# Kernel optimization log

Measured on AMD Instinct MI355X. Metric: run time of the kernel, lower is better.

Reference implementation:

```python
import jax, jax.numpy as jnp
import numpy as np

NUM_QUANTIZERS = 8
CODEBOOK_SIZE = 1024
DIM = 64
B, N = 8, 8192


def setup_inputs() -> dict:
    key = jax.random.key(0)
    kx, kc = jax.random.split(key)
    x = jax.random.normal(kx, (B, N, DIM), dtype=jnp.float32)
    # one codebook per quantizer stage (shared_codebook=False)
    codebooks = jax.random.normal(kc, (NUM_QUANTIZERS, CODEBOOK_SIZE, DIM), dtype=jnp.float32)
    return {"x": x, "codebooks": codebooks}


def reference(x, codebooks):
    """Residual VQ: sequential nearest-codebook lookup with residual subtraction.

    x:         [b, n, d]
    codebooks: [Q, K, d]
    returns quantized_out: [b, n, d]
    """

    def step(carry, cb):
        residual, qout = carry                       # [b,n,d], [b,n,d]
        # squared euclidean distances, [b,n,K]
        r_sq = jnp.sum(residual * residual, axis=-1, keepdims=True)
        c_sq = jnp.sum(cb * cb, axis=-1)             # [K]
        dots = jnp.einsum('bnd,kd->bnk', residual, cb)
        dist = r_sq - 2.0 * dots + c_sq              # [b,n,K]
        idx = jnp.argmin(dist, axis=-1)              # [b,n]
        quant = cb[idx]                              # [b,n,d] gather
        # straight-through estimator (VectorQuantize forward)
        quant_st = residual + jax.lax.stop_gradient(quant - residual)
        new_residual = residual - jax.lax.stop_gradient(quant)
        return (new_residual, qout + quant_st), idx

    init = (x, jnp.zeros_like(x))
    (residual, quantized_out), all_indices = jax.lax.scan(step, init, codebooks)
    return quantized_out
```

## Files before the change

kernel.cpp:

```cpp
#include <hip/hip_runtime.h>

#define NQ 8
#define KCODES 1024
#define D 64
#define CHUNK 64
#define NCHUNK 16
#define TPB 256
#define TOKPB 128
#define BIAS 96.0f

using short8 = __attribute__((ext_vector_type(8))) short;
using f32x4  = __attribute__((ext_vector_type(4))) float;

#define GLOBAL_AS __attribute__((address_space(1)))
#define LDS_AS    __attribute__((address_space(3)))

static __device__ __forceinline__ unsigned bf16_rne_bits(float f) {
    unsigned u = __float_as_uint(f);
    return (u + 0x7fffu + ((u >> 16) & 1u)) >> 16;
}
static __device__ __forceinline__ unsigned umn(unsigned a, unsigned b) { return a < b ? a : b; }
static __device__ __forceinline__ unsigned umx(unsigned a, unsigned b) { return a > b ? a : b; }
static __device__ __forceinline__ unsigned umed3(unsigned a, unsigned b, unsigned c) {
    return umx(umn(a, b), umn(umx(a, b), c));
}

__global__ __launch_bounds__(256) void prep_cb(const float* __restrict__ cb,
                                               int4* __restrict__ ws_cb) {
    int id = blockIdx.x * 256 + threadIdx.x;
    int n_rel = id & 63;
    int plane = (id >> 6) & 15;
    int ch    = (id >> 10) & 15;
    int q     = id >> 14;
    int g = plane & 3, kt = (plane >> 2) & 1, term = plane >> 3;
    int n = ch * CHUNK + n_rel;
    const float* src = cb + ((size_t)(q * KCODES + n)) * D + kt * 32 + g * 8;
    union { short s[8]; int4 v; } u;
    #pragma unroll
    for (int j = 0; j < 8; ++j) {
        float f = -src[j];
        unsigned hb = bf16_rne_bits(f);
        if (term == 0) {
            u.s[j] = (short)hb;
        } else {
            float lo = f - __uint_as_float(hb << 16);
            u.s[j] = (short)bf16_rne_bits(lo);
        }
    }
    ws_cb[id] = u.v;
}

__global__ __launch_bounds__(256) void prep_csq(const float* __restrict__ cb,
                                                float* __restrict__ ws_csq,
                                                float* __restrict__ ws_csqh) {
    int id = blockIdx.x * 256 + threadIdx.x;
    const float* c = cb + (size_t)id * D;
    float s0 = 0.f, s1 = 0.f, s2 = 0.f, s3 = 0.f;
    #pragma unroll
    for (int j = 0; j < 16; ++j) {
        s0 = fmaf(c[4*j+0], c[4*j+0], s0);
        s1 = fmaf(c[4*j+1], c[4*j+1], s1);
        s2 = fmaf(c[4*j+2], c[4*j+2], s2);
        s3 = fmaf(c[4*j+3], c[4*j+3], s3);
    }
    float cs = (s0 + s1) + (s2 + s3);
    ws_csq[id]  = cs;
    ws_csqh[id] = 0.5f * cs + BIAS;
}

__global__ __launch_bounds__(TPB, 4) void rvq_mfma(
    const float* __restrict__ x,
    const float* __restrict__ cb,
    const int4* __restrict__ ws_cb,
    const float* __restrict__ ws_csq,
    float* __restrict__ out)
{
    __shared__ __align__(16) int4  lds_stage[1024];
    __shared__ __align__(16) float lds_resid[TOKPB * 68];
    __shared__ float    lds_csqh[CHUNK];
    __shared__ unsigned lds_cand[TOKPB * 3];
    __shared__ int      lds_pick[TOKPB];

    const int tid  = threadIdx.x;
    const int lane = tid & 63;
    const int wave = tid >> 6;
    const int g    = lane >> 4;
    const int c    = lane & 15;
    const int tok0 = blockIdx.x * TOKPB;

    {
        const int t = tid >> 1, part = tid & 1;
        const float4* xp = (const float4*)(x + (size_t)(tok0 + t) * D + part * 32);
        float4* rr = (float4*)(lds_resid + t * 68 + part * 32);
        #pragma unroll
        for (int k2 = 0; k2 < 8; ++k2) rr[k2] = xp[k2];
    }

    const char* bp = (const char*)lds_stage + (c << 4) + (g << 10);

    for (int q = 0; q < NQ; ++q) {
        __syncthreads();

        short8 ah0[2], ah1[2], al0[2], al1[2];
        #pragma unroll
        for (int s = 0; s < 2; ++s) {
            const float* rr = lds_resid + (wave * 32 + s * 16 + c) * 68;
            float4 f0 = *(const float4*)(rr + 8 * g);
            float4 f1 = *(const float4*)(rr + 8 * g + 4);
            float4 f2 = *(const float4*)(rr + 32 + 8 * g);
            float4 f3 = *(const float4*)(rr + 36 + 8 * g);
            const float* v0 = (const float*)&f0;
            const float* v1 = (const float*)&f1;
            const float* v2 = (const float*)&f2;
            const float* v3 = (const float*)&f3;
            #pragma unroll
            for (int j = 0; j < 4; ++j) {
                float a = v0[j], b = v1[j], e = v2[j], f = v3[j];
                unsigned ha = bf16_rne_bits(a);
                unsigned hb = bf16_rne_bits(b);
                unsigned he = bf16_rne_bits(e);
                unsigned hf = bf16_rne_bits(f);
                ah0[s][j]   = (short)ha;  ah0[s][4+j] = (short)hb;
                ah1[s][j]   = (short)he;  ah1[s][4+j] = (short)hf;
                al0[s][j]   = (short)bf16_rne_bits(a - __uint_as_float(ha << 16));
                al0[s][4+j] = (short)bf16_rne_bits(b - __uint_as_float(hb << 16));
                al1[s][j]   = (short)bf16_rne_bits(e - __uint_as_float(he << 16));
                al1[s][4+j] = (short)bf16_rne_bits(f - __uint_as_float(hf << 16));
            }
        }

        unsigned T1[2][4], T2[2][4], T3[2][4];
        #pragma unroll
        for (int s = 0; s < 2; ++s)
            #pragma unroll
            for (int r = 0; r < 4; ++r) { T1[s][r] = 0xFFFFFFFFu; T2[s][r] = 0xFFFFFFFFu; T3[s][r] = 0xFFFFFFFFu; }

        for (int ch = 0; ch < NCHUNK; ++ch) {
            __syncthreads();
            {
                const int4* src = ws_cb + (size_t)(q * NCHUNK + ch) * 1024 + tid;
                LDS_AS char* ldst = (LDS_AS char*)lds_stage + tid * 16;
                #pragma unroll
                for (int t = 0; t < 4; ++t) {
                    __builtin_amdgcn_global_load_lds(
                        (const GLOBAL_AS unsigned int*)(src + t * 256),
                        (LDS_AS unsigned int*)(ldst + t * 4096), 16, 0, 0);
                }
                if (tid < CHUNK) {
                    __builtin_amdgcn_global_load_lds(
                        (const GLOBAL_AS unsigned int*)(ws_csq + 8192 + q * KCODES + ch * CHUNK + tid),
                        (LDS_AS unsigned int*)(&lds_csqh[tid]), 4, 0, 0);
                }
            }
            __syncthreads();

            #pragma unroll
            for (int tt = 0; tt < 4; ++tt) {
                short8 bh0 = *(const short8*)(bp + tt * 256);
                short8 bh1 = *(const short8*)(bp + 4096  + tt * 256);
                short8 bl0 = *(const short8*)(bp + 8192  + tt * 256);
                short8 bl1 = *(const short8*)(bp + 12288 + tt * 256);
                const float sd = lds_csqh[tt * 16 + c];
                const unsigned codev = (unsigned)(ch * CHUNK + tt * 16 + c);
                #pragma unroll
                for (int s = 0; s < 2; ++s) {
                    f32x4 acc = {sd, sd, sd, sd};
                    acc = __builtin_amdgcn_mfma_f32_16x16x32_bf16(ah0[s], bh0, acc, 0, 0, 0);
                    acc = __builtin_amdgcn_mfma_f32_16x16x32_bf16(ah1[s], bh1, acc, 0, 0, 0);
                    acc = __builtin_amdgcn_mfma_f32_16x16x32_bf16(al0[s], bh0, acc, 0, 0, 0);
                    acc = __builtin_amdgcn_mfma_f32_16x16x32_bf16(ah0[s], bl0, acc, 0, 0, 0);
                    acc = __builtin_amdgcn_mfma_f32_16x16x32_bf16(al1[s], bh1, acc, 0, 0, 0);
                    acc = __builtin_amdgcn_mfma_f32_16x16x32_bf16(ah1[s], bl1, acc, 0, 0, 0);
                    #pragma unroll
                    for (int r = 0; r < 4; ++r) {
                        unsigned p = (__float_as_uint(acc[r]) & 0xFFFFFC00u) | codev;
                        unsigned n2 = umn(T2[s][r], umx(T1[s][r], p));
                        unsigned n3 = umn(T3[s][r], umx(T2[s][r], p));
                        T1[s][r] = umn(T1[s][r], p);
                        T2[s][r] = n2;
                        T3[s][r] = n3;
                    }
                }
            }
        }

        #pragma unroll
        for (int st = 1; st <= 8; st <<= 1) {
            #pragma unroll
            for (int s = 0; s < 2; ++s) {
                #pragma unroll
                for (int r = 0; r < 4; ++r) {
                    unsigned o1 = (unsigned)__shfl_xor((int)T1[s][r], st);
                    unsigned o2 = (unsigned)__shfl_xor((int)T2[s][r], st);
                    unsigned o3 = (unsigned)__shfl_xor((int)T3[s][r], st);
                    unsigned x1 = umn(T1[s][r], o1), y1 = umx(T1[s][r], o1);
                    unsigned x2 = umn(T2[s][r], o2), y2 = umx(T2[s][r], o2);
                    unsigned x3 = umn(T3[s][r], o3);
                    T1[s][r] = x1;
                    T3[s][r] = umed3(y1, x2, umn(y2, x3));
                    T2[s][r] = umn(y1, x2);
                }
            }
        }

        if (c == 0) {
            #pragma unroll
            for (int s = 0; s < 2; ++s)
                #pragma unroll
                for (int r = 0; r < 4; ++r) {
                    const int idx = (wave * 32 + s * 16 + g * 4 + r) * 3;
                    lds_cand[idx + 0] = T1[s][r];
                    lds_cand[idx + 1] = T2[s][r];
                    lds_cand[idx + 2] = T3[s][r];
                }
        }
        __syncthreads();

        #pragma unroll
        for (int p = 0; p < 2; ++p) {
            const int t4  = lane >> 2;
            const int sel = lane & 3;
            const int row = wave * 32 + p * 16 + t4;
            const unsigned m1 = lds_cand[row * 3 + 0];
            const unsigned m2 = lds_cand[row * 3 + 1];
            const unsigned m3 = lds_cand[row * 3 + 2];
            const unsigned psel = (sel == 0) ? m1 : ((sel == 1) ? m2 : m3);
            const int cd = (int)(psel & 1023u);

            const float4* rrv = (const float4*)(lds_resid + row * 68);
            const float4* cpv = (const float4*)(cb + ((size_t)(q * KCODES + cd)) * D);
            float ax = 0.f, ay = 0.f, az = 0.f, aw = 0.f;
            #pragma unroll
            for (int j = 0; j < 16; ++j) {
                float4 rv = rrv[j];
                float4 cv = cpv[j];
                ax = fmaf(rv.x, cv.x, ax);
                ay = fmaf(rv.y, cv.y, ay);
                az = fmaf(rv.z, cv.z, az);
                aw = fmaf(rv.w, cv.w, aw);
            }
            float dot = (ax + ay) + (az + aw);
            float dd = fmaf(dot, -2.0f, ws_csq[q * KCODES + cd]);

            const int base = lane & ~3;
            float d0 = __shfl(dd, base);
            float d1 = __shfl(dd, base + 1);
            float d2 = __shfl(dd, base + 2);
            int cc0 = (int)(m1 & 1023u);
            int cc1 = (int)(m2 & 1023u);
            int cc2 = (int)(m3 & 1023u);
            float db = d0; int pick = cc0;
            if (d1 < db || (d1 == db && cc1 < pick)) { db = d1; pick = cc1; }
            if (d2 < db || (d2 == db && cc2 < pick)) { db = d2; pick = cc2; }
            if (sel == 0) lds_pick[row] = pick;
        }
        __syncthreads();

        {
            const int t = tid >> 1, part = tid & 1;
            const int ifin = lds_pick[t];
            const float4* cp = (const float4*)(cb + ((size_t)(q * KCODES + ifin)) * D + part * 32);
            float4* rr = (float4*)(lds_resid + t * 68 + part * 32);
            #pragma unroll
            for (int k2 = 0; k2 < 8; ++k2) {
                float4 rv = rr[k2], cv = cp[k2];
                rv.x -= cv.x; rv.y -= cv.y; rv.z -= cv.z; rv.w -= cv.w;
                rr[k2] = rv;
            }
        }
    }

    __syncthreads();
    {
        const int t = tid >> 1, part = tid & 1;
        const float4* xp = (const float4*)(x + (size_t)(tok0 + t) * D + part * 32);
        const float4* rr = (const float4*)(lds_resid + t * 68 + part * 32);
        float4* op = (float4*)(out + (size_t)(tok0 + t) * D + part * 32);
        #pragma unroll
        for (int k2 = 0; k2 < 8; ++k2) {
            float4 xv = xp[k2], rv = rr[k2];
            float4 o;
            o.x = xv.x - rv.x; o.y = xv.y - rv.y;
            o.z = xv.z - rv.z; o.w = xv.w - rv.w;
            op[k2] = o;
        }
    }
}

extern "C" void kernel_launch(void* const* d_in, const int* in_sizes, int n_in,
                              void* d_out, int out_size, void* d_ws, size_t ws_size,
                              hipStream_t stream) {
    const float* x  = (const float*)d_in[0];
    const float* cb = (const float*)d_in[1];
    float* out = (float*)d_out;

    int4*  ws_cb   = (int4*)d_ws;
    float* ws_csq  = (float*)((char*)d_ws + (size_t)2 * 1024 * 1024);
    float* ws_csqh = ws_csq + 8192;

    prep_cb <<<512, 256, 0, stream>>>(cb, ws_cb);
    prep_csq<<< 32, 256, 0, stream>>>(cb, ws_csq, ws_csqh);

    const int n_tokens = in_sizes[0] / D;
    const int grid = n_tokens / TOKPB;
    rvq_mfma<<<grid, TPB, 0, stream>>>(x, cb, ws_cb, ws_csq, out);
}
```

Before: 367.5 us.

## Halve tokens per block and split codebook chunk across wave pairs

Each block now handles 64 tokens instead of 128. Pairs of waves share the same 32 tokens, and each wave computes distances against half of every 64-code chunk. Per-half top-3 candidate lists are merged through LDS before the exact fp32 rescoring. This doubles the grid size to give more blocks for occupancy and latency hiding across CUs. In exchange, the codebook staging traffic per token doubles and a merge step is added.

```diff
diff --git a/kernel.cpp b/kernel.cpp
--- a/kernel.cpp
+++ b/kernel.cpp
@@ -6,7 +6,7 @@
 #define CHUNK 64
 #define NCHUNK 16
 #define TPB 256
-#define TOKPB 128
+#define TOKPB 64
 #define BIAS 96.0f
 
 using short8 = __attribute__((ext_vector_type(8))) short;
@@ -78,25 +78,27 @@
     __shared__ __align__(16) int4  lds_stage[1024];
     __shared__ __align__(16) float lds_resid[TOKPB * 68];
     __shared__ float    lds_csqh[CHUNK];
-    __shared__ unsigned lds_cand[TOKPB * 3];
+    __shared__ unsigned lds_cand[2][TOKPB * 3];
     __shared__ int      lds_pick[TOKPB];
 
-    const int tid  = threadIdx.x;
-    const int lane = tid & 63;
-    const int wave = tid >> 6;
-    const int g    = lane >> 4;
-    const int c    = lane & 15;
-    const int tok0 = blockIdx.x * TOKPB;
+    const int tid   = threadIdx.x;
+    const int lane  = tid & 63;
+    const int wave  = tid >> 6;
+    const int group = wave >> 1;
+    const int half  = wave & 1;
+    const int g     = lane >> 4;
+    const int c     = lane & 15;
+    const int tok0  = blockIdx.x * TOKPB;
 
     {
-        const int t = tid >> 1, part = tid & 1;
-        const float4* xp = (const float4*)(x + (size_t)(tok0 + t) * D + part * 32);
-        float4* rr = (float4*)(lds_resid + t * 68 + part * 32);
-        #pragma unroll
-        for (int k2 = 0; k2 < 8; ++k2) rr[k2] = xp[k2];
-    }
-
-    const char* bp = (const char*)lds_stage + (c << 4) + (g << 10);
+        const int t = tid >> 2, part = tid & 3;
+        const float4* xp = (const float4*)(x + (size_t)(tok0 + t) * D + part * 16);
+        float4* rr = (float4*)(lds_resid + t * 68 + part * 16);
+        #pragma unroll
+        for (int k2 = 0; k2 < 4; ++k2) rr[k2] = xp[k2];
+    }
+
+    const char* bp = (const char*)lds_stage + (c << 4) + (g << 10) + half * 512;
 
     for (int q = 0; q < NQ; ++q) {
         __syncthreads();
@@ -104,7 +106,7 @@
         short8 ah0[2], ah1[2], al0[2], al1[2];
         #pragma unroll
         for (int s = 0; s < 2; ++s) {
-            const float* rr = lds_resid + (wave * 32 + s * 16 + c) * 68;
+            const float* rr = lds_resid + (group * 32 + s * 16 + c) * 68;
             float4 f0 = *(const float4*)(rr + 8 * g);
             float4 f1 = *(const float4*)(rr + 8 * g + 4);
             float4 f2 = *(const float4*)(rr + 32 + 8 * g);
@@ -155,13 +157,13 @@
             __syncthreads();
 
             #pragma unroll
-            for (int tt = 0; tt < 4; ++tt) {
-                short8 bh0 = *(const short8*)(bp + tt * 256);
-                short8 bh1 = *(const short8*)(bp + 4096  + tt * 256);
-                short8 bl0 = *(const short8*)(bp + 8192  + tt * 256);
-                short8 bl1 = *(const short8*)(bp + 12288 + tt * 256);
-                const float sd = lds_csqh[tt * 16 + c];
-                const unsigned codev = (unsigned)(ch * CHUNK + tt * 16 + c);
+            for (int i = 0; i < 2; ++i) {
+                short8 bh0 = *(const short8*)(bp + i * 256);
+                short8 bh1 = *(const short8*)(bp + 4096  + i * 256);
+                short8 bl0 = *(const short8*)(bp + 8192  + i * 256);
+                short8 bl1 = *(const short8*)(bp + 12288 + i * 256);
+                const float sd = lds_csqh[(half * 2 + i) * 16 + c];
+                const unsigned codev = (unsigned)(ch * CHUNK + (half * 2 + i) * 16 + c);
                 #pragma unroll
                 for (int s = 0; s < 2; ++s) {
                     f32x4 acc = {sd, sd, sd, sd};
@@ -208,22 +210,30 @@
             for (int s = 0; s < 2; ++s)
                 #pragma unroll
                 for (int r = 0; r < 4; ++r) {
-                    const int idx = (wave * 32 + s * 16 + g * 4 + r) * 3;
-                    lds_cand[idx + 0] = T1[s][r];
-                    lds_cand[idx + 1] = T2[s][r];
-                    lds_cand[idx + 2] = T3[s][r];
+                    const int idx = (group * 32 + s * 16 + g * 4 + r) * 3;
+                    lds_cand[half][idx + 0] = T1[s][r];
+                    lds_cand[half][idx + 1] = T2[s][r];
+                    lds_cand[half][idx + 2] = T3[s][r];
                 }
         }
         __syncthreads();
 
-        #pragma unroll
-        for (int p = 0; p < 2; ++p) {
+        {
             const int t4  = lane >> 2;
             const int sel = lane & 3;
-            const int row = wave * 32 + p * 16 + t4;
-            const unsigned m1 = lds_cand[row * 3 + 0];
-            const unsigned m2 = lds_cand[row * 3 + 1];
-            const unsigned m3 = lds_cand[row * 3 + 2];
+            const int row = group * 32 + half * 16 + t4;
+            unsigned a1 = lds_cand[0][row * 3 + 0];
+            unsigned a2 = lds_cand[0][row * 3 + 1];
+            unsigned a3 = lds_cand[0][row * 3 + 2];
+            unsigned b1 = lds_cand[1][row * 3 + 0];
+            unsigned b2 = lds_cand[1][row * 3 + 1];
+            unsigned b3 = lds_cand[1][row * 3 + 2];
+            unsigned x1 = umn(a1, b1), y1 = umx(a1, b1);
+            unsigned x2 = umn(a2, b2), y2 = umx(a2, b2);
+            unsigned x3 = umn(a3, b3);
+            unsigned m1 = x1;
+            unsigned m2 = umn(y1, x2);
+            unsigned m3 = umed3(y1, x2, umn(y2, x3));
             const unsigned psel = (sel == 0) ? m1 : ((sel == 1) ? m2 : m3);
             const int cd = (int)(psel & 1023u);
 
@@ -257,12 +267,12 @@
         __syncthreads();
 
         {
-            const int t = tid >> 1, part = tid & 1;
+            const int t = tid >> 2, part = tid & 3;
             const int ifin = lds_pick[t];
-            const float4* cp = (const float4*)(cb + ((size_t)(q * KCODES + ifin)) * D + part * 32);
-            float4* rr = (float4*)(lds_resid + t * 68 + part * 32);
-            #pragma unroll
-            for (int k2 = 0; k2 < 8; ++k2) {
+            const float4* cp = (const float4*)(cb + ((size_t)(q * KCODES + ifin)) * D + part * 16);
+            float4* rr = (float4*)(lds_resid + t * 68 + part * 16);
+            #pragma unroll
+            for (int k2 = 0; k2 < 4; ++k2) {
                 float4 rv = rr[k2], cv = cp[k2];
                 rv.x -= cv.x; rv.y -= cv.y; rv.z -= cv.z; rv.w -= cv.w;
                 rr[k2] = rv;
@@ -272,12 +282,12 @@
 
     __syncthreads();
     {
-        const int t = tid >> 1, part = tid & 1;
-        const float4* xp = (const float4*)(x + (size_t)(tok0 + t) * D + part * 32);
-        const float4* rr = (const float4*)(lds_resid + t * 68 + part * 32);
-        float4* op = (float4*)(out + (size_t)(tok0 + t) * D + part * 32);
-        #pragma unroll
-        for (int k2 = 0; k2 < 8; ++k2) {
+        const int t = tid >> 2, part = tid & 3;
+        const float4* xp = (const float4*)(x + (size_t)(tok0 + t) * D + part * 16);
+        const float4* rr = (const float4*)(lds_resid + t * 68 + part * 16);
+        float4* op = (float4*)(out + (size_t)(tok0 + t) * D + part * 16);
+        #pragma unroll
+        for (int k2 = 0; k2 < 4; ++k2) {
             float4 xv = xp[k2], rv = rr[k2];
             float4 o;
             o.x = xv.x - rv.x; o.y = xv.y - rv.y;
```

New measurement: 352.2 us. 4.1% less time.
